# Kernel optimization log

Measured on AMD Instinct MI355X. Metric: run time of the kernel, lower is better.

Reference implementation:

```python
import jax, jax.numpy as jnp
import numpy as np

B, P, F = 128, 4096, 32
K, D = 8, 64
ITERS = 2
EPS_ATTN = 1e-8
EPS_LN = 1e-5
SCALE = D ** -0.5


def _layernorm(x, g, b):
    mu = jnp.mean(x, axis=-1, keepdims=True)
    var = jnp.mean((x - mu) ** 2, axis=-1, keepdims=True)
    return (x - mu) * jax.lax.rsqrt(var + EPS_LN) * g + b


def setup_inputs() -> dict:
    key = jax.random.key(0)
    ks = jax.random.split(key, 16)
    s = lambda fan_in: 1.0 / np.sqrt(fan_in)
    inp = {
        "x": jax.random.normal(ks[0], (B, P, F), dtype=jnp.float32),
        "noise": jax.random.normal(ks[1], (B, K, D), dtype=jnp.float32),
        "slots_mu": jax.random.normal(ks[2], (1, 1, D), dtype=jnp.float32),
        "slots_sigma": jnp.ones((1, 1, D), dtype=jnp.float32) * 0.1,
        # torch Linear weights: [out, in]
        "Wq": jax.random.uniform(ks[3], (D, D), jnp.float32, -s(D), s(D)),
        "Wk": jax.random.uniform(ks[4], (D, F), jnp.float32, -s(F), s(F)),
        "Wv": jax.random.uniform(ks[5], (D, F), jnp.float32, -s(F), s(F)),
        # GRUCell params: weight_ih/[3D,D], weight_hh/[3D,D], biases [3D]
        "W_ih": jax.random.uniform(ks[6], (3 * D, D), jnp.float32, -s(D), s(D)),
        "W_hh": jax.random.uniform(ks[7], (3 * D, D), jnp.float32, -s(D), s(D)),
        "b_ih": jax.random.uniform(ks[8], (3 * D,), jnp.float32, -s(D), s(D)),
        "b_hh": jax.random.uniform(ks[9], (3 * D,), jnp.float32, -s(D), s(D)),
        "ln_in_g": jnp.ones((F,), jnp.float32),
        "ln_in_b": jnp.zeros((F,), jnp.float32),
        "ln_slots_g": jnp.ones((D,), jnp.float32),
        "ln_slots_b": jnp.zeros((D,), jnp.float32),
        "ff_ln_g": jnp.ones((D,), jnp.float32),
        "ff_ln_b": jnp.zeros((D,), jnp.float32),
        "ff_W1": jax.random.uniform(ks[10], (2 * D, D), jnp.float32, -s(D), s(D)),
        "ff_b1": jax.random.uniform(ks[11], (2 * D,), jnp.float32, -s(D), s(D)),
        "ff_W2": jax.random.uniform(ks[12], (D, 2 * D), jnp.float32, -s(2 * D), s(2 * D)),
        "ff_b2": jax.random.uniform(ks[13], (D,), jnp.float32, -s(2 * D), s(2 * D)),
    }
    return inp


def _gru_cell(x, h, W_ih, W_hh, b_ih, b_hh):
    # x, h: [N, D]
    gi = x @ W_ih.T + b_ih  # [N, 3D]
    gh = h @ W_hh.T + b_hh
    i_r, i_z, i_n = jnp.split(gi, 3, axis=-1)
    h_r, h_z, h_n = jnp.split(gh, 3, axis=-1)
    r = jax.nn.sigmoid(i_r + h_r)
    z = jax.nn.sigmoid(i_z + h_z)
    n = jnp.tanh(i_n + r * h_n)
    return (1.0 - z) * n + z * h


def reference(x, noise, slots_mu, slots_sigma, Wq, Wk, Wv, W_ih, W_hh, b_ih, b_hh,
              ln_in_g, ln_in_b, ln_slots_g, ln_slots_b,
              ff_ln_g, ff_ln_b, ff_W1, ff_b1, ff_W2, ff_b2):
    x_norm = _layernorm(x, ln_in_g, ln_in_b)          # [B,P,F]
    k = x_norm @ Wk.T                                  # [B,P,D]
    v = x_norm @ Wv.T                                  # [B,P,D]
    slots = slots_mu + jnp.abs(slots_sigma) * noise    # [B,K,D]
    last_attn = None
    for _ in range(ITERS):
        slots_prev = slots
        q = _layernorm(slots, ln_slots_g, ln_slots_b) @ Wq.T  # [B,K,D]
        dots = jnp.einsum('bkd,bpd->bkp', q, k) * SCALE       # [B,K,P]
        attn = jax.nn.softmax(dots, axis=1) + EPS_ATTN        # softmax over slots
        attn = attn / jnp.sum(attn, axis=-1, keepdims=True)   # normalize over pixels
        last_attn = attn
        updates = jnp.einsum('bkp,bpd->bkd', attn, v)         # [B,K,D]
        h = _gru_cell(updates.reshape(-1, D), slots_prev.reshape(-1, D),
                      W_ih, W_hh, b_ih, b_hh).reshape(x.shape[0], K, D)
        ff_in = _layernorm(h, ff_ln_g, ff_ln_b)
        ff_out = jax.nn.relu(ff_in @ ff_W1.T + ff_b1) @ ff_W2.T + ff_b2
        slots = h + ff_out
    return slots, last_attn
```

## Files before the change

kernel.cpp:

```cpp
#include <hip/hip_runtime.h>
#include <hip/hip_bf16.h>
#include <stdint.h>

#define Bb 128
#define Pp 4096
#define Ff 32
#define Kk 8
#define Dd 64

constexpr float EPS_ATTN_ = 1e-8f;
constexpr float EPS_LN_   = 1e-5f;
constexpr float SCALE_    = 0.125f;

typedef __attribute__((ext_vector_type(8))) short short8;
typedef __attribute__((ext_vector_type(4))) float floatx4;
typedef __attribute__((ext_vector_type(4))) unsigned uintx4;

__device__ __forceinline__ unsigned short f2bf(float f) {
  union { float f; unsigned u; } c; c.f = f;
  unsigned u = c.u + 0x7fffu + ((c.u >> 16) & 1u);
  return (unsigned short)(u >> 16);
}
__device__ __forceinline__ float bf2f(unsigned h) {
  union { float f; unsigned u; } c; c.u = h << 16;
  return c.f;
}
__device__ __forceinline__ unsigned pkbf(float a, float b) {
  __hip_bfloat162 h2 = __float22bfloat162_rn(make_float2(a, b));
  union { __hip_bfloat162 h; unsigned u; } c; c.h = h2;
  return c.u;
}
__device__ __forceinline__ float wsum(float v) {
  v += __shfl_xor(v, 1, 64);  v += __shfl_xor(v, 2, 64);
  v += __shfl_xor(v, 4, 64);  v += __shfl_xor(v, 8, 64);
  v += __shfl_xor(v, 16, 64); v += __shfl_xor(v, 32, 64);
  return v;
}

#define ROUNDS 2
template <bool FIRST>
__global__ __launch_bounds__(256) void fattn_kernel(
    const float* __restrict__ x, const unsigned short* __restrict__ qt_bf,
    const float* __restrict__ lg, const float* __restrict__ lb,
    const float* __restrict__ noise, const float* __restrict__ smu,
    const float* __restrict__ ssig, const float* __restrict__ Wq,
    const float* __restrict__ Wk, const float* __restrict__ lsg,
    const float* __restrict__ lsb,
    float* __restrict__ acc_tp, float* __restrict__ Ssp,
    unsigned short* __restrict__ attn_bf) {
  const int b  = blockIdx.x;
  const int w    = threadIdx.x >> 6;
  const int lane = threadIdx.x & 63;
  const int m    = lane & 15;
  const int quad = lane >> 4;
  __shared__ __align__(16) char smem[41984];
  float* xs = (float*)smem;
  unsigned short* xb  = (unsigned short*)smem;
  unsigned short* xbT = (unsigned short*)(smem + 20480);
  unsigned short (*A_lds)[8][72] = (unsigned short (*)[8][72])(smem + 37376);

  short8 aq;
  if (FIRST) {
    float* wq  = (float*)smem;
    float* wk  = (float*)(smem + 16640);
    float* lnv = (float*)(smem + 25088);
    unsigned short* qtb = (unsigned short*)(smem + 27136);
    {
      const float4* g4 = (const float4*)Wq;
      #pragma unroll
      for (int i = 0; i < 4; ++i) {
        int f4i = threadIdx.x + i * 256;
        float4 v = g4[f4i];
        int fi = f4i * 4, row = fi >> 6, col = fi & 63;
        float* dst = &wq[row * 65 + col];
        dst[0] = v.x; dst[1] = v.y; dst[2] = v.z; dst[3] = v.w;
      }
      const float4* gk = (const float4*)Wk;
      #pragma unroll
      for (int i = 0; i < 2; ++i) {
        int f4i = threadIdx.x + i * 256;
        float4 v = gk[f4i];
        int fi = f4i * 4, row = fi >> 5, col = fi & 31;
        float* dst = &wk[row * 33 + col];
        dst[0] = v.x; dst[1] = v.y; dst[2] = v.z; dst[3] = v.w;
      }
    }
    const int j = lane;
    #pragma unroll
    for (int kk0 = 0; kk0 < 2; ++kk0) {
      const int kk = w + kk0 * 4;
      float s0 = smu[j] + fabsf(ssig[j]) * noise[((size_t)b * Kk + kk) * Dd + j];
      float mu  = wsum(s0) * (1.f / 64.f);
      float dc  = s0 - mu;
      float var = wsum(dc * dc) * (1.f / 64.f);
      lnv[kk * 64 + j] = dc * rsqrtf(var + EPS_LN_) * lsg[j] + lsb[j];
    }
    __syncthreads();
    float qa = 0.f, qb = 0.f;
    #pragma unroll 8
    for (int d = 0; d < Dd; ++d) {
      float wv = wq[j * 65 + d];
      qa = fmaf(wv, lnv[w * 64 + d],       qa);
      qb = fmaf(wv, lnv[(w + 4) * 64 + d], qb);
    }
    __syncthreads();
    lnv[w * 64 + j]       = qa * SCALE_;
    lnv[(w + 4) * 64 + j] = qb * SCALE_;
    __syncthreads();
    {
      const int kq = threadIdx.x >> 5, fq = threadIdx.x & 31;
      float qt = 0.f;
      #pragma unroll 8
      for (int d = 0; d < Dd; ++d) qt = fmaf(lnv[kq * 64 + d], wk[d * 33 + fq], qt);
      qtb[kq * 32 + fq]       = f2bf(qt);
      qtb[(kq + 8) * 32 + fq] = 0;
    }
    __syncthreads();
    aq = *(const short8*)&qtb[m * 32 + quad * 8];
    __syncthreads();
  } else {
    aq = *(const short8*)(qt_bf + ((size_t)b * 16 + m) * Ff + quad * 8);
  }

  float Ss0 = 0.f, Ss1 = 0.f, Ss2 = 0.f, Ss3 = 0.f;
  floatx4 Cg0 = {0.f,0.f,0.f,0.f}, Cg1 = {0.f,0.f,0.f,0.f};

  for (int rr = 0; rr < ROUNDS; ++rr) {
    const int p0 = (blockIdx.y * ROUNDS + rr) * 256;
    if (rr) __syncthreads();
    {
      const float4* xg4 = (const float4*)(x + ((size_t)b * Pp + p0) * Ff);
      float4 st[8];
      #pragma unroll
      for (int i = 0; i < 8; ++i) st[i] = xg4[threadIdx.x + i * 256];
      #pragma unroll
      for (int i = 0; i < 8; ++i) {
        int f4i = threadIdx.x + i * 256;
        int px = f4i >> 3, c = (f4i & 7) * 4;
        *(float4*)&xs[px * 36 + c] = st[i];
      }
    }
    __syncthreads();
    unsigned pku[16];
    {
      float xv[Ff];
      #pragma unroll
      for (int j4 = 0; j4 < 8; ++j4) {
        float4 t = *(const float4*)&xs[threadIdx.x * 36 + j4 * 4];
        xv[j4*4] = t.x; xv[j4*4+1] = t.y; xv[j4*4+2] = t.z; xv[j4*4+3] = t.w;
      }
      float mu = 0.f;
      #pragma unroll
      for (int j = 0; j < Ff; ++j) mu += xv[j];
      mu *= (1.f / Ff);
      float var = 0.f;
      #pragma unroll
      for (int j = 0; j < Ff; ++j) { float d = xv[j] - mu; var = fmaf(d, d, var); }
      var *= (1.f / Ff);
      float rn = rsqrtf(var + EPS_LN_);
      #pragma unroll
      for (int j = 0; j < Ff; ++j) xv[j] = (xv[j] - mu) * rn * lg[j] + lb[j];
      #pragma unroll
      for (int p = 0; p < 16; ++p) pku[p] = pkbf(xv[2 * p], xv[2 * p + 1]);
    }
    __syncthreads();
    #pragma unroll
    for (int j8 = 0; j8 < 4; ++j8)
      *(uintx4*)&xb[threadIdx.x * 40 + j8 * 8] = *(uintx4*)&pku[j8 * 4];
    #pragma unroll
    for (int p = 0; p < 16; ++p) {
      xbT[(2 * p)     * 264 + threadIdx.x] = (unsigned short)(pku[p] & 0xffffu);
      xbT[(2 * p + 1) * 264 + threadIdx.x] = (unsigned short)(pku[p] >> 16);
    }
    __syncthreads();

    #pragma unroll
    for (int t = 0; t < 4; ++t) {
      const int lpx = w * 64 + t * 16 + m;
      const short8 bx = *(const short8*)&xb[lpx * 40 + quad * 8];
      floatx4 C = {0.f, 0.f, 0.f, 0.f};
      C = __builtin_amdgcn_mfma_f32_16x16x32_bf16(aq, bx, C, 0, 0, 0);
      float mx = fmaxf(fmaxf(C[0], C[1]), fmaxf(C[2], C[3]));
      mx = fmaxf(mx, __shfl_xor(mx, 16, 64));
      float e0 = __expf(C[0] - mx), e1 = __expf(C[1] - mx),
            e2 = __expf(C[2] - mx), e3 = __expf(C[3] - mx);
      float s = e0 + e1 + e2 + e3;
      s += __shfl_xor(s, 16, 64);
      float inv = 1.f / s;
      float a0 = fmaf(e0, inv, EPS_ATTN_), a1 = fmaf(e1, inv, EPS_ATTN_);
      float a2 = fmaf(e2, inv, EPS_ATTN_), a3 = fmaf(e3, inv, EPS_ATTN_);
      Ss0 += a0; Ss1 += a1; Ss2 += a2; Ss3 += a3;
      if (quad < 2) {
        const int r0 = quad * 4;
        unsigned c01 = pkbf(a0, a1), c23 = pkbf(a2, a3);
        A_lds[w][r0 + 0][t * 16 + m] = (unsigned short)(c01 & 0xffffu);
        A_lds[w][r0 + 1][t * 16 + m] = (unsigned short)(c01 >> 16);
        A_lds[w][r0 + 2][t * 16 + m] = (unsigned short)(c23 & 0xffffu);
        A_lds[w][r0 + 3][t * 16 + m] = (unsigned short)(c23 >> 16);
        if (!FIRST) {
          unsigned short* ao = attn_bf + ((size_t)b * Kk + r0) * Pp + p0 + w * 64 + t * 16 + m;
          ao[0]      = (unsigned short)(c01 & 0xffffu);
          ao[Pp]     = (unsigned short)(c01 >> 16);
          ao[2 * Pp] = (unsigned short)(c23 & 0xffffu);
          ao[3 * Pp] = (unsigned short)(c23 >> 16);
        }
      }
    }
    __syncthreads();
    #pragma unroll
    for (int ks = 0; ks < 2; ++ks) {
      const short8 af = *(const short8*)(&A_lds[w][m & 7][ks * 32 + quad * 8]);
      const int pxo = w * 64 + ks * 32 + quad * 8;
      const short8 xg0 = *(const short8*)&xbT[(m)      * 264 + pxo];
      const short8 xg1 = *(const short8*)&xbT[(16 + m) * 264 + pxo];
      Cg0 = __builtin_amdgcn_mfma_f32_16x16x32_bf16(af, xg0, Cg0, 0, 0, 0);
      Cg1 = __builtin_amdgcn_mfma_f32_16x16x32_bf16(af, xg1, Cg1, 0, 0, 0);
    }
  }
  Ss0 += __shfl_xor(Ss0,1,64); Ss0 += __shfl_xor(Ss0,2,64); Ss0 += __shfl_xor(Ss0,4,64); Ss0 += __shfl_xor(Ss0,8,64);
  Ss1 += __shfl_xor(Ss1,1,64); Ss1 += __shfl_xor(Ss1,2,64); Ss1 += __shfl_xor(Ss1,4,64); Ss1 += __shfl_xor(Ss1,8,64);
  Ss2 += __shfl_xor(Ss2,1,64); Ss2 += __shfl_xor(Ss2,2,64); Ss2 += __shfl_xor(Ss2,4,64); Ss2 += __shfl_xor(Ss2,8,64);
  Ss3 += __shfl_xor(Ss3,1,64); Ss3 += __shfl_xor(Ss3,2,64); Ss3 += __shfl_xor(Ss3,4,64); Ss3 += __shfl_xor(Ss3,8,64);
  if (quad < 2) {
    const int row = quad * 4;
    const int slice = blockIdx.y * 4 + w;
    float* tp = acc_tp + (size_t)b * 8192 + (size_t)slice * 256 + (size_t)row * 32 + m;
    #pragma unroll
    for (int r = 0; r < 4; ++r) {
      tp[r * 32]      = Cg0[r];
      tp[r * 32 + 16] = Cg1[r];
    }
    if (m == 0) {
      float* sp = Ssp + ((size_t)b * 32 + slice) * 8 + row;
      sp[0] = Ss0; sp[1] = Ss1; sp[2] = Ss2; sp[3] = Ss3;
    }
  }
}

template <bool LAST>
__global__ __launch_bounds__(256) void gru_kernel(
    const float* __restrict__ acc_tp, const float* __restrict__ Ssp,
    float* __restrict__ slots,
    const float* __restrict__ noise, const float* __restrict__ smu,
    const float* __restrict__ ssig,
    const float* __restrict__ W_ih, const float* __restrict__ W_hh,
    const float* __restrict__ b_ih, const float* __restrict__ b_hh,
    const float* __restrict__ fg, const float* __restrict__ fb,
    const float* __restrict__ W1, const float* __restrict__ b1,
    const float* __restrict__ W2, const float* __restrict__ b2,
    const float* __restrict__ lsg, const float* __restrict__ lsb,
    const float* __restrict__ Wq, const float* __restrict__ Wv,
    const float* __restrict__ Wk,
    unsigned short* __restrict__ qt_bf,
    float* __restrict__ out_slots) {
  const int b = blockIdx.x;
  const int kh = blockIdx.y;
  const int k = threadIdx.x >> 6;
  const int j = threadIdx.x & 63;
  const int kg = kh * 4 + k;
  __shared__ float WA[192 * 65];
  __shared__ float WB[192 * 65];
  __shared__ float WVs[64 * 33];
  __shared__ float WKs[64 * 33];
  __shared__ float At[4][Ff];
  __shared__ float Ub[4][Dd];
  __shared__ float Hb[4][Dd];
  __shared__ float Tb[4][2 * Dd];
  __shared__ float qs[4][Dd];
  {
    const float4* gi = (const float4*)W_ih;
    const float4* gh = (const float4*)W_hh;
    #pragma unroll
    for (int i = 0; i < 12; ++i) {
      int f4i = threadIdx.x + i * 256;
      float4 vi = gi[f4i], vh = gh[f4i];
      int fi = f4i * 4, row = fi >> 6, col = fi & 63;
      float* da = &WA[row * 65 + col];
      float* db = &WB[row * 65 + col];
      da[0]=vi.x; da[1]=vi.y; da[2]=vi.z; da[3]=vi.w;
      db[0]=vh.x; db[1]=vh.y; db[2]=vh.z; db[3]=vh.w;
    }
    const float4* gv = (const float4*)Wv;
    #pragma unroll
    for (int i = 0; i < 2; ++i) {
      int f4i = threadIdx.x + i * 256;
      float4 v = gv[f4i];
      int fi = f4i * 4, row = fi >> 5, col = fi & 31;
      float* d_ = &WVs[row * 33 + col];
      d_[0]=v.x; d_[1]=v.y; d_[2]=v.z; d_[3]=v.w;
    }
    if (!LAST) {
      const float4* gk = (const float4*)Wk;
      #pragma unroll
      for (int i = 0; i < 2; ++i) {
        int f4i = threadIdx.x + i * 256;
        float4 v = gk[f4i];
        int fi = f4i * 4, row = fi >> 5, col = fi & 31;
        float* d_ = &WKs[row * 33 + col];
        d_[0]=v.x; d_[1]=v.y; d_[2]=v.z; d_[3]=v.w;
      }
    }
  }
  const size_t rk = (size_t)b * Kk + kg;
  float S = 0.f;
  #pragma unroll
  for (int y = 0; y < 32; ++y) S += Ssp[((size_t)b * 32 + y) * 8 + kg];
  if (j < Ff) {
    const float* tp = acc_tp + (size_t)b * 8192 + (size_t)kg * 32 + j;
    float t = 0.f;
    #pragma unroll
    for (int y = 0; y < 32; ++y) t += tp[y * 256];
    At[k][j] = t;
  }
  float h;
  if (LAST) h = slots[rk * Dd + j];
  else      h = smu[j] + fabsf(ssig[j]) * noise[rk * Dd + j];
  Hb[k][j] = h;
  __syncthreads();
  float u = 0.f;
  #pragma unroll 8
  for (int f = 0; f < Ff; ++f) u = fmaf(WVs[j * 33 + f], At[k][f], u);
  u /= S;
  Ub[k][j] = u;
  __syncthreads();
  float gr = b_ih[j], gz = b_ih[64 + j], gn = b_ih[128 + j];
  float hr = b_hh[j], hz = b_hh[64 + j], hn_ = b_hh[128 + j];
  #pragma unroll 4
  for (int d = 0; d < Dd; ++d) {
    const float ud = Ub[k][d], hd = Hb[k][d];
    gr  = fmaf(WA[j * 65 + d],         ud, gr);
    gz  = fmaf(WA[(64 + j) * 65 + d],  ud, gz);
    gn  = fmaf(WA[(128 + j) * 65 + d], ud, gn);
    hr  = fmaf(WB[j * 65 + d],         hd, hr);
    hz  = fmaf(WB[(64 + j) * 65 + d],  hd, hz);
    hn_ = fmaf(WB[(128 + j) * 65 + d], hd, hn_);
  }
  const float r = 1.f / (1.f + __expf(-(gr + hr)));
  const float z = 1.f / (1.f + __expf(-(gz + hz)));
  const float n = tanhf(fmaf(r, hn_, gn));
  const float hnew = fmaf(z, h - n, n);
  float mu  = wsum(hnew) * (1.f / 64.f);
  float dc  = hnew - mu;
  float var = wsum(dc * dc) * (1.f / 64.f);
  float fi_ = dc * rsqrtf(var + EPS_LN_) * fg[j] + fb[j];
  __syncthreads();
  Ub[k][j] = fi_;
  {
    const float4* g1 = (const float4*)W1;
    #pragma unroll
    for (int i = 0; i < 8; ++i) {
      int f4i = threadIdx.x + i * 256;
      float4 v = g1[f4i];
      int fi = f4i * 4, row = fi >> 6, col = fi & 63;
      float* d_ = &WA[row * 65 + col];
      d_[0]=v.x; d_[1]=v.y; d_[2]=v.z; d_[3]=v.w;
    }
    if (!LAST) {
      const float4* gq = (const float4*)Wq;
      #pragma unroll
      for (int i = 0; i < 4; ++i) {
        int f4i = threadIdx.x + i * 256;
        float4 v = gq[f4i];
        int fi = f4i * 4, row = fi >> 6, col = fi & 63;
        float* d_ = &WA[8320 + row * 65 + col];
        d_[0]=v.x; d_[1]=v.y; d_[2]=v.z; d_[3]=v.w;
      }
    }
    const float4* g2 = (const float4*)W2;
    #pragma unroll
    for (int i = 0; i < 8; ++i) {
      int f4i = threadIdx.x + i * 256;
      float4 v = g2[f4i];
      int fi = f4i * 4, row = fi >> 7, col = fi & 127;
      float* d_ = &WB[row * 129 + col];
      d_[0]=v.x; d_[1]=v.y; d_[2]=v.z; d_[3]=v.w;
    }
  }
  __syncthreads();
  float f1a = b1[j], f1b = b1[64 + j];
  #pragma unroll 4
  for (int d = 0; d < Dd; ++d) {
    const float t = Ub[k][d];
    f1a = fmaf(WA[j * 65 + d],        t, f1a);
    f1b = fmaf(WA[(64 + j) * 65 + d], t, f1b);
  }
  f1a = fmaxf(f1a, 0.f);
  f1b = fmaxf(f1b, 0.f);
  Tb[k][j]      = f1a;
  Tb[k][64 + j] = f1b;
  __syncthreads();
  float o = b2[j];
  #pragma unroll 4
  for (int e = 0; e < 2 * Dd; ++e) o = fmaf(WB[j * 129 + e], Tb[k][e], o);
  const float sn = hnew + o;
  if (!LAST) {
    slots[rk * Dd + j] = sn;
    float mq = wsum(sn) * (1.f / 64.f);
    float dq = sn - mq;
    float vq = wsum(dq * dq) * (1.f / 64.f);
    float xq = dq * rsqrtf(vq + EPS_LN_) * lsg[j] + lsb[j];
    Ub[k][j] = xq;
    __syncthreads();
    float q = 0.f;
    #pragma unroll 8
    for (int d = 0; d < Dd; ++d) q = fmaf(WA[8320 + j * 65 + d], Ub[k][d], q);
    qs[k][j] = q * SCALE_;
    __syncthreads();
    if (j < Ff) {
      float qt = 0.f;
      #pragma unroll 8
      for (int d = 0; d < Dd; ++d) qt = fmaf(qs[k][d], WKs[d * 33 + j], qt);
      qt_bf[((size_t)b * 16 + kg) * Ff + j]     = f2bf(qt);
      qt_bf[((size_t)b * 16 + kg + 8) * Ff + j] = 0;
    }
  } else {
    out_slots[rk * Dd + j] = sn;
  }
}

__global__ __launch_bounds__(256) void scale_kernel(
    const float* __restrict__ Ssp, const unsigned short* __restrict__ attn_bf,
    float* __restrict__ out_attn) {
  const size_t idx = ((size_t)blockIdx.x * 256 + threadIdx.x) * 4;
  const int bk = (int)(idx >> 12);
  const int b = bk >> 3, k = bk & 7;
  float S = 0.f;
  #pragma unroll
  for (int y = 0; y < 32; ++y) S += Ssp[((size_t)b * 32 + y) * 8 + k];
  const float inv = 1.f / S;
  uint2 v = *(const uint2*)(attn_bf + idx);
  float4 o;
  o.x = bf2f(v.x & 0xffffu) * inv;
  o.y = bf2f(v.x >> 16)     * inv;
  o.z = bf2f(v.y & 0xffffu) * inv;
  o.w = bf2f(v.y >> 16)     * inv;
  *(float4*)(out_attn + idx) = o;
}

extern "C" void kernel_launch(void* const* d_in, const int* in_sizes, int n_in,
                              void* d_out, int out_size, void* d_ws, size_t ws_size,
                              hipStream_t stream) {
  const float* x      = (const float*)d_in[0];
  const float* noise  = (const float*)d_in[1];
  const float* smu    = (const float*)d_in[2];
  const float* ssig   = (const float*)d_in[3];
  const float* Wq     = (const float*)d_in[4];
  const float* Wk     = (const float*)d_in[5];
  const float* Wv     = (const float*)d_in[6];
  const float* W_ih   = (const float*)d_in[7];
  const float* W_hh   = (const float*)d_in[8];
  const float* b_ih   = (const float*)d_in[9];
  const float* b_hh   = (const float*)d_in[10];
  const float* ln_in_g = (const float*)d_in[11];
  const float* ln_in_b = (const float*)d_in[12];
  const float* ln_s_g  = (const float*)d_in[13];
  const float* ln_s_b  = (const float*)d_in[14];
  const float* ff_g   = (const float*)d_in[15];
  const float* ff_b   = (const float*)d_in[16];
  const float* W1     = (const float*)d_in[17];
  const float* b1     = (const float*)d_in[18];
  const float* W2     = (const float*)d_in[19];
  const float* b2     = (const float*)d_in[20];

  char* ws = (char*)d_ws;
  unsigned short* qt_bf = (unsigned short*)(ws);
  float* slots   = (float*)(ws + 131072);
  float* acc_tp  = (float*)(ws + 393216);
  float* Ssp     = (float*)(ws + 4587520);
  unsigned short* attn_bf = (unsigned short*)(ws + 4718592);

  float* out_slots = (float*)d_out;
  float* out_attn  = out_slots + (size_t)Bb * Kk * Dd;

  fattn_kernel<true><<<dim3(Bb, 8), dim3(256), 0, stream>>>(
      x, qt_bf, ln_in_g, ln_in_b, noise, smu, ssig, Wq, Wk, ln_s_g, ln_s_b,
      acc_tp, Ssp, nullptr);
  gru_kernel<false><<<dim3(Bb, 2), dim3(256), 0, stream>>>(
      acc_tp, Ssp, slots, noise, smu, ssig, W_ih, W_hh, b_ih, b_hh, ff_g, ff_b,
      W1, b1, W2, b2, ln_s_g, ln_s_b, Wq, Wv, Wk, qt_bf, nullptr);
  fattn_kernel<false><<<dim3(Bb, 8), dim3(256), 0, stream>>>(
      x, qt_bf, ln_in_g, ln_in_b, nullptr, nullptr, nullptr, nullptr, nullptr,
      nullptr, nullptr, acc_tp, Ssp, attn_bf);
  gru_kernel<true><<<dim3(Bb, 2), dim3(256), 0, stream>>>(
      acc_tp, Ssp, slots, noise, smu, ssig, W_ih, W_hh, b_ih, b_hh, ff_g, ff_b,
      W1, b1, W2, b2, ln_s_g, ln_s_b, Wq, Wv, Wk, qt_bf, out_slots);
  scale_kernel<<<dim3(4096), dim3(256), 0, stream>>>(Ssp, attn_bf, out_attn);
}
```

Measured before the change: 200.1 us.

## Fuse all phases into persistent megakernel with grid barriers and register prefetch

Replaces the five separate launches (two attention passes, two GRU passes, scale) with one persistent kernel of 256 blocks that moves between phases using atomic-counter grid barriers. Each attention block now covers 2048 pixels over 8 rounds and prefetches the next round of x into registers while it computes the current one. The last prefetch of the first pass preloads round 0 for the second pass. The GRU phase streams its gate weights into a smaller shared-memory footprint so the phases can share one buffer. The aim is to remove launch gaps and hide global-load latency. The cost is lower occupancy (one 4-wave block per CU), spin-wait barriers that assume every block is co-resident, and an extra memset launch.

```diff
diff --git a/kernel.cpp b/kernel.cpp
--- a/kernel.cpp
+++ b/kernel.cpp
@@ -7,6 +7,9 @@
 #define Ff 32
 #define Kk 8
 #define Dd 64
+#define ROUNDS 8
+#define NSLICE 8
+#define NBLOCKS 256
 
 constexpr float EPS_ATTN_ = 1e-8f;
 constexpr float EPS_LN_   = 1e-5f;
@@ -37,9 +40,24 @@
   return v;
 }
 
-#define ROUNDS 2
-template <bool FIRST>
-__global__ __launch_bounds__(256) void fattn_kernel(
+__device__ __forceinline__ void gbar(unsigned* c) {
+  __syncthreads();
+  if (threadIdx.x == 0) {
+    __threadfence();
+    atomicAdd(c, 1u);
+    while (__hip_atomic_load(c, __ATOMIC_RELAXED,
+                             __HIP_MEMORY_SCOPE_AGENT) < (unsigned)NBLOCKS) {
+      __builtin_amdgcn_s_sleep(2);
+    }
+    __threadfence();
+  }
+  __syncthreads();
+}
+
+
+template <bool ITER2, bool PRE>
+__device__ void fattn_phase(
+    char* smem, float4 (&st)[8],
     const float* __restrict__ x, const unsigned short* __restrict__ qt_bf,
     const float* __restrict__ lg, const float* __restrict__ lb,
     const float* __restrict__ noise, const float* __restrict__ smu,
@@ -48,19 +66,26 @@
     const float* __restrict__ lsb,
     float* __restrict__ acc_tp, float* __restrict__ Ssp,
     unsigned short* __restrict__ attn_bf) {
-  const int b  = blockIdx.x;
+  const int b    = blockIdx.x;
+  const int yb   = blockIdx.y;
   const int w    = threadIdx.x >> 6;
   const int lane = threadIdx.x & 63;
   const int m    = lane & 15;
   const int quad = lane >> 4;
-  __shared__ __align__(16) char smem[41984];
   float* xs = (float*)smem;
   unsigned short* xb  = (unsigned short*)smem;
   unsigned short* xbT = (unsigned short*)(smem + 20480);
   unsigned short (*A_lds)[8][72] = (unsigned short (*)[8][72])(smem + 37376);
 
+  const float4* xg4 =
+      (const float4*)(x + ((size_t)b * Pp + (size_t)yb * (ROUNDS * 256)) * Ff);
+  if (!PRE) {
+    #pragma unroll
+    for (int i = 0; i < 8; ++i) st[i] = xg4[threadIdx.x + i * 256];
+  }
+
   short8 aq;
-  if (FIRST) {
+  if (!ITER2) {
     float* wq  = (float*)smem;
     float* wk  = (float*)(smem + 16640);
     float* lnv = (float*)(smem + 25088);
@@ -125,20 +150,14 @@
   float Ss0 = 0.f, Ss1 = 0.f, Ss2 = 0.f, Ss3 = 0.f;
   floatx4 Cg0 = {0.f,0.f,0.f,0.f}, Cg1 = {0.f,0.f,0.f,0.f};
 
+  #pragma unroll 1
   for (int rr = 0; rr < ROUNDS; ++rr) {
-    const int p0 = (blockIdx.y * ROUNDS + rr) * 256;
     if (rr) __syncthreads();
-    {
-      const float4* xg4 = (const float4*)(x + ((size_t)b * Pp + p0) * Ff);
-      float4 st[8];
-      #pragma unroll
-      for (int i = 0; i < 8; ++i) st[i] = xg4[threadIdx.x + i * 256];
-      #pragma unroll
-      for (int i = 0; i < 8; ++i) {
-        int f4i = threadIdx.x + i * 256;
-        int px = f4i >> 3, c = (f4i & 7) * 4;
-        *(float4*)&xs[px * 36 + c] = st[i];
-      }
+    #pragma unroll
+    for (int i = 0; i < 8; ++i) {
+      int f4i = threadIdx.x + i * 256;
+      int px = f4i >> 3, c = (f4i & 7) * 4;
+      *(float4*)&xs[px * 36 + c] = st[i];
     }
     __syncthreads();
     unsigned pku[16];
@@ -163,6 +182,14 @@
       #pragma unroll
       for (int p = 0; p < 16; ++p) pku[p] = pkbf(xv[2 * p], xv[2 * p + 1]);
     }
+    {
+      const bool more = (rr + 1 < ROUNDS);
+      if (more || !ITER2) {
+        const float4* xn = xg4 + (size_t)2048 * (more ? (rr + 1) : 0);
+        #pragma unroll
+        for (int i = 0; i < 8; ++i) st[i] = xn[threadIdx.x + i * 256];
+      }
+    }
     __syncthreads();
     #pragma unroll
     for (int j8 = 0; j8 < 4; ++j8)
@@ -174,6 +201,7 @@
     }
     __syncthreads();
 
+    const int p0 = yb * (ROUNDS * 256) + rr * 256;
     #pragma unroll
     for (int t = 0; t < 4; ++t) {
       const int lpx = w * 64 + t * 16 + m;
@@ -197,8 +225,9 @@
         A_lds[w][r0 + 1][t * 16 + m] = (unsigned short)(c01 >> 16);
         A_lds[w][r0 + 2][t * 16 + m] = (unsigned short)(c23 & 0xffffu);
         A_lds[w][r0 + 3][t * 16 + m] = (unsigned short)(c23 >> 16);
-        if (!FIRST) {
-          unsigned short* ao = attn_bf + ((size_t)b * Kk + r0) * Pp + p0 + w * 64 + t * 16 + m;
+        if (ITER2) {
+          unsigned short* ao =
+              attn_bf + ((size_t)b * Kk + r0) * Pp + p0 + w * 64 + t * 16 + m;
           ao[0]      = (unsigned short)(c01 & 0xffffu);
           ao[Pp]     = (unsigned short)(c01 >> 16);
           ao[2 * Pp] = (unsigned short)(c23 & 0xffffu);
@@ -223,22 +252,40 @@
   Ss3 += __shfl_xor(Ss3,1,64); Ss3 += __shfl_xor(Ss3,2,64); Ss3 += __shfl_xor(Ss3,4,64); Ss3 += __shfl_xor(Ss3,8,64);
   if (quad < 2) {
     const int row = quad * 4;
-    const int slice = blockIdx.y * 4 + w;
-    float* tp = acc_tp + (size_t)b * 8192 + (size_t)slice * 256 + (size_t)row * 32 + m;
+    const int slice = yb * 4 + w;
+    float* tp = acc_tp + (size_t)b * (NSLICE * 256) + (size_t)slice * 256 +
+                (size_t)row * 32 + m;
     #pragma unroll
     for (int r = 0; r < 4; ++r) {
       tp[r * 32]      = Cg0[r];
       tp[r * 32 + 16] = Cg1[r];
     }
     if (m == 0) {
-      float* sp = Ssp + ((size_t)b * 32 + slice) * 8 + row;
+      float* sp = Ssp + ((size_t)b * NSLICE + slice) * 8 + row;
       sp[0] = Ss0; sp[1] = Ss1; sp[2] = Ss2; sp[3] = Ss3;
     }
   }
 }
 
+__device__ __forceinline__ void stage_gate_pair(
+    float* A, float* Bd, const float* Wih, const float* Whh, int g) {
+  const float4* gi = (const float4*)Wih + (size_t)g * 1024;
+  const float4* gh = (const float4*)Whh + (size_t)g * 1024;
+  #pragma unroll
+  for (int i = 0; i < 4; ++i) {
+    int f4i = threadIdx.x + i * 256;
+    float4 vi = gi[f4i], vh = gh[f4i];
+    int fi = f4i * 4, row = fi >> 6, col = fi & 63;
+    float* da = &A[row * 65 + col];
+    float* db = &Bd[row * 65 + col];
+    da[0]=vi.x; da[1]=vi.y; da[2]=vi.z; da[3]=vi.w;
+    db[0]=vh.x; db[1]=vh.y; db[2]=vh.z; db[3]=vh.w;
+  }
+}
+
 template <bool LAST>
-__global__ __launch_bounds__(256) void gru_kernel(
+__device__ void gru_phase(
+    char* smem,
     const float* __restrict__ acc_tp, const float* __restrict__ Ssp,
     float* __restrict__ slots,
     const float* __restrict__ noise, const float* __restrict__ smu,
@@ -251,89 +298,81 @@
     const float* __restrict__ lsg, const float* __restrict__ lsb,
     const float* __restrict__ Wq, const float* __restrict__ Wv,
     const float* __restrict__ Wk,
-    unsigned short* __restrict__ qt_bf,
-    float* __restrict__ out_slots) {
-  const int b = blockIdx.x;
+    unsigned short* __restrict__ qt_bf, float* __restrict__ out_slots) {
+  const int b  = blockIdx.x;
   const int kh = blockIdx.y;
-  const int k = threadIdx.x >> 6;
-  const int j = threadIdx.x & 63;
+  const int k  = threadIdx.x >> 6;
+  const int j  = threadIdx.x & 63;
   const int kg = kh * 4 + k;
-  __shared__ float WA[192 * 65];
-  __shared__ float WB[192 * 65];
-  __shared__ float WVs[64 * 33];
-  __shared__ float WKs[64 * 33];
-  __shared__ float At[4][Ff];
-  __shared__ float Ub[4][Dd];
-  __shared__ float Hb[4][Dd];
-  __shared__ float Tb[4][2 * Dd];
-  __shared__ float qs[4][Dd];
+  const size_t rk = (size_t)b * Kk + kg;
+  float* WS0 = (float*)smem;
+  float* At  = (float*)(smem + 16640);
+  float* WS1 = (float*)(smem + 16640);
+  float* qs  = (float*)(smem + 16640);
+  float* WKs = (float*)(smem + 17664);
+  float* Ub  = (float*)(smem + 33280);
+  float* Hb  = (float*)(smem + 34304);
+  float* Tb  = (float*)(smem + 35328);
+
   {
-    const float4* gi = (const float4*)W_ih;
-    const float4* gh = (const float4*)W_hh;
-    #pragma unroll
-    for (int i = 0; i < 12; ++i) {
-      int f4i = threadIdx.x + i * 256;
-      float4 vi = gi[f4i], vh = gh[f4i];
-      int fi = f4i * 4, row = fi >> 6, col = fi & 63;
-      float* da = &WA[row * 65 + col];
-      float* db = &WB[row * 65 + col];
-      da[0]=vi.x; da[1]=vi.y; da[2]=vi.z; da[3]=vi.w;
-      db[0]=vh.x; db[1]=vh.y; db[2]=vh.z; db[3]=vh.w;
-    }
     const float4* gv = (const float4*)Wv;
     #pragma unroll
     for (int i = 0; i < 2; ++i) {
       int f4i = threadIdx.x + i * 256;
       float4 v = gv[f4i];
       int fi = f4i * 4, row = fi >> 5, col = fi & 31;
-      float* d_ = &WVs[row * 33 + col];
+      float* d_ = &WS0[row * 33 + col];
       d_[0]=v.x; d_[1]=v.y; d_[2]=v.z; d_[3]=v.w;
     }
-    if (!LAST) {
-      const float4* gk = (const float4*)Wk;
-      #pragma unroll
-      for (int i = 0; i < 2; ++i) {
-        int f4i = threadIdx.x + i * 256;
-        float4 v = gk[f4i];
-        int fi = f4i * 4, row = fi >> 5, col = fi & 31;
-        float* d_ = &WKs[row * 33 + col];
-        d_[0]=v.x; d_[1]=v.y; d_[2]=v.z; d_[3]=v.w;
-      }
-    }
-  }
-  const size_t rk = (size_t)b * Kk + kg;
+  }
   float S = 0.f;
   #pragma unroll
-  for (int y = 0; y < 32; ++y) S += Ssp[((size_t)b * 32 + y) * 8 + kg];
+  for (int y2 = 0; y2 < NSLICE; ++y2) S += Ssp[((size_t)b * NSLICE + y2) * 8 + kg];
   if (j < Ff) {
-    const float* tp = acc_tp + (size_t)b * 8192 + (size_t)kg * 32 + j;
+    const float* tp = acc_tp + (size_t)b * (NSLICE * 256) + (size_t)kg * 32 + j;
     float t = 0.f;
     #pragma unroll
-    for (int y = 0; y < 32; ++y) t += tp[y * 256];
-    At[k][j] = t;
+    for (int y2 = 0; y2 < NSLICE; ++y2) t += tp[y2 * 256];
+    At[k * Ff + j] = t;
   }
   float h;
   if (LAST) h = slots[rk * Dd + j];
   else      h = smu[j] + fabsf(ssig[j]) * noise[rk * Dd + j];
-  Hb[k][j] = h;
+  Hb[k * Dd + j] = h;
   __syncthreads();
   float u = 0.f;
   #pragma unroll 8
-  for (int f = 0; f < Ff; ++f) u = fmaf(WVs[j * 33 + f], At[k][f], u);
+  for (int f = 0; f < Ff; ++f) u = fmaf(WS0[j * 33 + f], At[k * Ff + f], u);
   u /= S;
-  Ub[k][j] = u;
-  __syncthreads();
-  float gr = b_ih[j], gz = b_ih[64 + j], gn = b_ih[128 + j];
-  float hr = b_hh[j], hz = b_hh[64 + j], hn_ = b_hh[128 + j];
+  Ub[k * Dd + j] = u;
+  __syncthreads();
+
+  float gr, hr, gz, hz, gn, hn_;
+  stage_gate_pair(WS0, WS1, W_ih, W_hh, 0);
+  __syncthreads();
+  gr = b_ih[j]; hr = b_hh[j];
   #pragma unroll 4
   for (int d = 0; d < Dd; ++d) {
-    const float ud = Ub[k][d], hd = Hb[k][d];
-    gr  = fmaf(WA[j * 65 + d],         ud, gr);
-    gz  = fmaf(WA[(64 + j) * 65 + d],  ud, gz);
-    gn  = fmaf(WA[(128 + j) * 65 + d], ud, gn);
-    hr  = fmaf(WB[j * 65 + d],         hd, hr);
-    hz  = fmaf(WB[(64 + j) * 65 + d],  hd, hz);
-    hn_ = fmaf(WB[(128 + j) * 65 + d], hd, hn_);
+    gr = fmaf(WS0[j * 65 + d], Ub[k * Dd + d], gr);
+    hr = fmaf(WS1[j * 65 + d], Hb[k * Dd + d], hr);
+  }
+  __syncthreads();
+  stage_gate_pair(WS0, WS1, W_ih, W_hh, 1);
+  __syncthreads();
+  gz = b_ih[64 + j]; hz = b_hh[64 + j];
+  #pragma unroll 4
+  for (int d = 0; d < Dd; ++d) {
+    gz = fmaf(WS0[j * 65 + d], Ub[k * Dd + d], gz);
+    hz = fmaf(WS1[j * 65 + d], Hb[k * Dd + d], hz);
+  }
+  __syncthreads();
+  stage_gate_pair(WS0, WS1, W_ih, W_hh, 2);
+  __syncthreads();
+  gn = b_ih[128 + j]; hn_ = b_hh[128 + j];
+  #pragma unroll 4
+  for (int d = 0; d < Dd; ++d) {
+    gn  = fmaf(WS0[j * 65 + d], Ub[k * Dd + d], gn);
+    hn_ = fmaf(WS1[j * 65 + d], Hb[k * Dd + d], hn_);
   }
   const float r = 1.f / (1.f + __expf(-(gr + hr)));
   const float z = 1.f / (1.f + __expf(-(gz + hz)));
@@ -344,7 +383,7 @@
   float var = wsum(dc * dc) * (1.f / 64.f);
   float fi_ = dc * rsqrtf(var + EPS_LN_) * fg[j] + fb[j];
   __syncthreads();
-  Ub[k][j] = fi_;
+  Ub[k * Dd + j] = fi_;
   {
     const float4* g1 = (const float4*)W1;
     #pragma unroll
@@ -352,46 +391,38 @@
       int f4i = threadIdx.x + i * 256;
       float4 v = g1[f4i];
       int fi = f4i * 4, row = fi >> 6, col = fi & 63;
-      float* d_ = &WA[row * 65 + col];
+      float* d_ = &WS0[row * 65 + col];
       d_[0]=v.x; d_[1]=v.y; d_[2]=v.z; d_[3]=v.w;
     }
-    if (!LAST) {
-      const float4* gq = (const float4*)Wq;
-      #pragma unroll
-      for (int i = 0; i < 4; ++i) {
-        int f4i = threadIdx.x + i * 256;
-        float4 v = gq[f4i];
-        int fi = f4i * 4, row = fi >> 6, col = fi & 63;
-        float* d_ = &WA[8320 + row * 65 + col];
-        d_[0]=v.x; d_[1]=v.y; d_[2]=v.z; d_[3]=v.w;
-      }
-    }
+  }
+  __syncthreads();
+  float f1a = b1[j], f1b = b1[64 + j];
+  #pragma unroll 4
+  for (int d = 0; d < Dd; ++d) {
+    const float t = Ub[k * Dd + d];
+    f1a = fmaf(WS0[j * 65 + d],        t, f1a);
+    f1b = fmaf(WS0[(64 + j) * 65 + d], t, f1b);
+  }
+  f1a = fmaxf(f1a, 0.f);
+  f1b = fmaxf(f1b, 0.f);
+  Tb[k * 128 + j]      = f1a;
+  Tb[k * 128 + 64 + j] = f1b;
+  __syncthreads();
+  {
     const float4* g2 = (const float4*)W2;
     #pragma unroll
     for (int i = 0; i < 8; ++i) {
       int f4i = threadIdx.x + i * 256;
       float4 v = g2[f4i];
       int fi = f4i * 4, row = fi >> 7, col = fi & 127;
-      float* d_ = &WB[row * 129 + col];
+      float* d_ = &WS0[row * 129 + col];
       d_[0]=v.x; d_[1]=v.y; d_[2]=v.z; d_[3]=v.w;
     }
   }
-  __syncthreads();
-  float f1a = b1[j], f1b = b1[64 + j];
-  #pragma unroll 4
-  for (int d = 0; d < Dd; ++d) {
-    const float t = Ub[k][d];
-    f1a = fmaf(WA[j * 65 + d],        t, f1a);
-    f1b = fmaf(WA[(64 + j) * 65 + d], t, f1b);
-  }
-  f1a = fmaxf(f1a, 0.f);
-  f1b = fmaxf(f1b, 0.f);
-  Tb[k][j]      = f1a;
-  Tb[k][64 + j] = f1b;
   __syncthreads();
   float o = b2[j];
   #pragma unroll 4
-  for (int e = 0; e < 2 * Dd; ++e) o = fmaf(WB[j * 129 + e], Tb[k][e], o);
+  for (int e = 0; e < 2 * Dd; ++e) o = fmaf(WS0[j * 129 + e], Tb[k * 128 + e], o);
   const float sn = hnew + o;
   if (!LAST) {
     slots[rk * Dd + j] = sn;
@@ -399,17 +430,38 @@
     float dq = sn - mq;
     float vq = wsum(dq * dq) * (1.f / 64.f);
     float xq = dq * rsqrtf(vq + EPS_LN_) * lsg[j] + lsb[j];
-    Ub[k][j] = xq;
+    __syncthreads();
+    Ub[k * Dd + j] = xq;
+    {
+      const float4* gq = (const float4*)Wq;
+      #pragma unroll
+      for (int i = 0; i < 4; ++i) {
+        int f4i = threadIdx.x + i * 256;
+        float4 v = gq[f4i];
+        int fi = f4i * 4, row = fi >> 6, col = fi & 63;
+        float* d_ = &WS0[row * 65 + col];
+        d_[0]=v.x; d_[1]=v.y; d_[2]=v.z; d_[3]=v.w;
+      }
+      const float4* gk2 = (const float4*)Wk;
+      #pragma unroll
+      for (int i = 0; i < 2; ++i) {
+        int f4i = threadIdx.x + i * 256;
+        float4 v = gk2[f4i];
+        int fi = f4i * 4, row = fi >> 5, col = fi & 31;
+        float* d_ = &WKs[row * 33 + col];
+        d_[0]=v.x; d_[1]=v.y; d_[2]=v.z; d_[3]=v.w;
+      }
+    }
     __syncthreads();
     float q = 0.f;
     #pragma unroll 8
-    for (int d = 0; d < Dd; ++d) q = fmaf(WA[8320 + j * 65 + d], Ub[k][d], q);
-    qs[k][j] = q * SCALE_;
+    for (int d = 0; d < Dd; ++d) q = fmaf(WS0[j * 65 + d], Ub[k * Dd + d], q);
+    qs[k * Dd + j] = q * SCALE_;
     __syncthreads();
     if (j < Ff) {
       float qt = 0.f;
       #pragma unroll 8
-      for (int d = 0; d < Dd; ++d) qt = fmaf(qs[k][d], WKs[d * 33 + j], qt);
+      for (int d = 0; d < Dd; ++d) qt = fmaf(qs[k * Dd + d], WKs[d * 33 + j], qt);
       qt_bf[((size_t)b * 16 + kg) * Ff + j]     = f2bf(qt);
       qt_bf[((size_t)b * 16 + kg + 8) * Ff + j] = 0;
     }
@@ -418,23 +470,67 @@
   }
 }
 
-__global__ __launch_bounds__(256) void scale_kernel(
-    const float* __restrict__ Ssp, const unsigned short* __restrict__ attn_bf,
-    float* __restrict__ out_attn) {
-  const size_t idx = ((size_t)blockIdx.x * 256 + threadIdx.x) * 4;
-  const int bk = (int)(idx >> 12);
-  const int b = bk >> 3, k = bk & 7;
-  float S = 0.f;
-  #pragma unroll
-  for (int y = 0; y < 32; ++y) S += Ssp[((size_t)b * 32 + y) * 8 + k];
-  const float inv = 1.f / S;
-  uint2 v = *(const uint2*)(attn_bf + idx);
-  float4 o;
-  o.x = bf2f(v.x & 0xffffu) * inv;
-  o.y = bf2f(v.x >> 16)     * inv;
-  o.z = bf2f(v.y & 0xffffu) * inv;
-  o.w = bf2f(v.y >> 16)     * inv;
-  *(float4*)(out_attn + idx) = o;
+__global__ __launch_bounds__(256) void mega_kernel(
+    const float* __restrict__ x, const float* __restrict__ noise,
+    const float* __restrict__ smu, const float* __restrict__ ssig,
+    const float* __restrict__ Wq, const float* __restrict__ Wk,
+    const float* __restrict__ Wv,
+    const float* __restrict__ W_ih, const float* __restrict__ W_hh,
+    const float* __restrict__ b_ih, const float* __restrict__ b_hh,
+    const float* __restrict__ lg, const float* __restrict__ lb,
+    const float* __restrict__ lsg, const float* __restrict__ lsb,
+    const float* __restrict__ fg, const float* __restrict__ fb,
+    const float* __restrict__ W1, const float* __restrict__ b1,
+    const float* __restrict__ W2, const float* __restrict__ b2,
+    unsigned short* __restrict__ qt_bf, float* __restrict__ slots,
+    float* __restrict__ acc_tp, float* __restrict__ Ssp,
+    unsigned short* __restrict__ attn_bf, unsigned* __restrict__ bar,
+    float* __restrict__ out_slots, float* __restrict__ out_attn) {
+  __shared__ __align__(16) char smem[41984];
+  float4 st[8];
+
+  fattn_phase<false, false>(smem, st, x, nullptr, lg, lb, noise, smu, ssig,
+                            Wq, Wk, lsg, lsb, acc_tp, Ssp, nullptr);
+  gbar(bar + 0);
+  gru_phase<false>(smem, acc_tp, Ssp, slots, noise, smu, ssig, W_ih, W_hh,
+                   b_ih, b_hh, fg, fb, W1, b1, W2, b2, lsg, lsb, Wq, Wv, Wk,
+                   qt_bf, nullptr);
+  gbar(bar + 1);
+  fattn_phase<true, true>(smem, st, x, qt_bf, lg, lb, nullptr, nullptr, nullptr,
+                          nullptr, nullptr, nullptr, nullptr, acc_tp, Ssp,
+                          attn_bf);
+  gbar(bar + 2);
+  {
+    const int b = blockIdx.x, yb = blockIdx.y;
+    float* Sbuf = (float*)smem;
+    if (threadIdx.x < 8) {
+      float S = 0.f;
+      #pragma unroll
+      for (int y2 = 0; y2 < NSLICE; ++y2)
+        S += Ssp[((size_t)b * NSLICE + y2) * 8 + threadIdx.x];
+      Sbuf[threadIdx.x] = 1.f / S;
+    }
+    __syncthreads();
+    #pragma unroll
+    for (int i = 0; i < 16; ++i) {
+      int idx = threadIdx.x + i * 256;
+      int slot = idx >> 9;
+      int px = (idx & 511) * 4;
+      size_t off = ((size_t)b * Kk + slot) * Pp + (size_t)yb * 2048 + px;
+      uint2 v = *(const uint2*)(attn_bf + off);
+      float inv = Sbuf[slot];
+      float4 ov;
+      ov.x = bf2f(v.x & 0xffffu) * inv;
+      ov.y = bf2f(v.x >> 16)     * inv;
+      ov.z = bf2f(v.y & 0xffffu) * inv;
+      ov.w = bf2f(v.y >> 16)     * inv;
+      *(float4*)(out_attn + off) = ov;
+    }
+  }
+  __syncthreads();
+  gru_phase<true>(smem, acc_tp, Ssp, slots, noise, smu, ssig, W_ih, W_hh,
+                  b_ih, b_hh, fg, fb, W1, b1, W2, b2, lsg, lsb, Wq, Wv, Wk,
+                  qt_bf, out_slots);
 }
 
 extern "C" void kernel_launch(void* const* d_in, const int* in_sizes, int n_in,
@@ -466,23 +562,16 @@
   unsigned short* qt_bf = (unsigned short*)(ws);
   float* slots   = (float*)(ws + 131072);
   float* acc_tp  = (float*)(ws + 393216);
-  float* Ssp     = (float*)(ws + 4587520);
-  unsigned short* attn_bf = (unsigned short*)(ws + 4718592);
+  float* Ssp     = (float*)(ws + 1441792);
+  unsigned short* attn_bf = (unsigned short*)(ws + 1474560);
+  unsigned* bar  = (unsigned*)(ws + 9863168);
 
   float* out_slots = (float*)d_out;
   float* out_attn  = out_slots + (size_t)Bb * Kk * Dd;
 
-  fattn_kernel<true><<<dim3(Bb, 8), dim3(256), 0, stream>>>(
-      x, qt_bf, ln_in_g, ln_in_b, noise, smu, ssig, Wq, Wk, ln_s_g, ln_s_b,
-      acc_tp, Ssp, nullptr);
-  gru_kernel<false><<<dim3(Bb, 2), dim3(256), 0, stream>>>(
-      acc_tp, Ssp, slots, noise, smu, ssig, W_ih, W_hh, b_ih, b_hh, ff_g, ff_b,
-      W1, b1, W2, b2, ln_s_g, ln_s_b, Wq, Wv, Wk, qt_bf, nullptr);
-  fattn_kernel<false><<<dim3(Bb, 8), dim3(256), 0, stream>>>(
-      x, qt_bf, ln_in_g, ln_in_b, nullptr, nullptr, nullptr, nullptr, nullptr,
-      nullptr, nullptr, acc_tp, Ssp, attn_bf);
-  gru_kernel<true><<<dim3(Bb, 2), dim3(256), 0, stream>>>(
-      acc_tp, Ssp, slots, noise, smu, ssig, W_ih, W_hh, b_ih, b_hh, ff_g, ff_b,
-      W1, b1, W2, b2, ln_s_g, ln_s_b, Wq, Wv, Wk, qt_bf, out_slots);
-  scale_kernel<<<dim3(4096), dim3(256), 0, stream>>>(Ssp, attn_bf, out_attn);
-}
+  hipMemsetAsync(bar, 0, 16, stream);
+  mega_kernel<<<dim3(Bb, 2), dim3(256), 0, stream>>>(
+      x, noise, smu, ssig, Wq, Wk, Wv, W_ih, W_hh, b_ih, b_hh,
+      ln_in_g, ln_in_b, ln_s_g, ln_s_b, ff_g, ff_b, W1, b1, W2, b2,
+      qt_bf, slots, acc_tp, Ssp, attn_bf, bar, out_slots, out_attn);
+}
```

After: 305.3 us. +52.6%, slower.
